# Kernel optimization log

Hardware: AMD Instinct MI355X
Metric: run time of the kernel (lower is better)

Reference implementation:

```python
import jax, jax.numpy as jnp
import numpy as np

B, N, F = 512, 64, 64
ROBOT_DIM, HUMAN_DIM, HID = 9, 5, 128
K = 3  # Chebyshev order


def setup_inputs() -> dict:
    key = jax.random.key(0)
    ks = jax.random.split(key, 16)
    # complete directed graph without self loops, shared across the batch
    src, dst = np.nonzero(~np.eye(N, dtype=bool))
    edge_index = jnp.asarray(np.stack([src, dst]), dtype=jnp.int32)  # [2, E]
    s = 0.05
    return {
        "robot_x": jax.random.normal(ks[0], (B, 1, ROBOT_DIM), jnp.float32),
        "human_x": jax.random.normal(ks[1], (B, N - 1, HUMAN_DIM), jnp.float32),
        "edge_index": edge_index,
        "wr1_w": jax.random.normal(ks[2], (ROBOT_DIM, HID), jnp.float32) * s,
        "wr1_b": jax.random.normal(ks[3], (HID,), jnp.float32) * s,
        "wr2_w": jax.random.normal(ks[4], (HID, F), jnp.float32) * s,
        "wr2_b": jax.random.normal(ks[5], (F,), jnp.float32) * s,
        "wh1_w": jax.random.normal(ks[6], (HUMAN_DIM, HID), jnp.float32) * s,
        "wh1_b": jax.random.normal(ks[7], (HID,), jnp.float32) * s,
        "wh2_w": jax.random.normal(ks[8], (HID, F), jnp.float32) * s,
        "wh2_b": jax.random.normal(ks[9], (F,), jnp.float32) * s,
        "cheb_w": jax.random.normal(ks[10], (K, F, F), jnp.float32) * s,
        "cheb_b": jax.random.normal(ks[11], (F,), jnp.float32) * s,
    }


def reference(robot_x, human_x, edge_index, wr1_w, wr1_b, wr2_w, wr2_b,
              wh1_w, wh1_b, wh2_w, wh2_b, cheb_w, cheb_b):
    # MLP embeddings with last_relu=True
    r = jax.nn.relu(robot_x @ wr1_w + wr1_b)
    r = jax.nn.relu(r @ wr2_w + wr2_b)            # [B, 1, F]
    h = jax.nn.relu(human_x @ wh1_w + wh1_b)
    h = jax.nn.relu(h @ wh2_w + wh2_b)            # [B, N-1, F]
    X = jnp.concatenate([r, h], axis=1)           # [B, N, F]

    src, dst = edge_index[0], edge_index[1]
    n = X.shape[1]
    # PyG ChebConv sym-normalized scaled Laplacian with lambda_max=2:
    # L_hat = -D^{-1/2} A D^{-1/2}  (edge weights all ones, no self loops)
    deg = jax.ops.segment_sum(jnp.ones(src.shape[0], X.dtype), src, num_segments=n)
    dinv = jnp.where(deg > 0, deg ** -0.5, 0.0)
    w = -(dinv[src] * dinv[dst])                  # [E]

    def prop(x):  # x: [B, N, F] -> L_hat @ x per batch via gather/scatter
        msg = x[:, src, :] * w[None, :, None]     # [B, E, F]
        return jnp.zeros_like(x).at[:, dst, :].add(msg)

    Tx0 = X
    Tx1 = prop(X)
    Tx2 = 2.0 * prop(Tx1) - Tx0
    Tx = jnp.stack([Tx0, Tx1, Tx2], axis=0)       # [K, B, N, F]
    out = jnp.einsum("kbnf,kfo->bno", Tx, cheb_w) + cheb_b
    return out[:, 0, :]                           # robot node output [B, F]
```

## Files before the change

kernel.cpp:

```cpp
#include <hip/hip_runtime.h>


#define BDIM 256

typedef __attribute__((ext_vector_type(8))) short bf16x8;
typedef __attribute__((ext_vector_type(4))) float f32x4;

static __device__ __forceinline__ unsigned short f2bf(float f) {
    unsigned int u = __float_as_uint(f);
    u += 0x7FFF + ((u >> 16) & 1);
    return (unsigned short)(u >> 16);
}

__global__ __launch_bounds__(256, 2) void dgcrnn_mfma(
    const float* __restrict__ robot_x,
    const float* __restrict__ human_x,
    const float* __restrict__ wr1, const float* __restrict__ wr1_b,
    const float* __restrict__ wr2, const float* __restrict__ wr2_b,
    const float* __restrict__ wh1, const float* __restrict__ wh1_b,
    const float* __restrict__ wh2, const float* __restrict__ wh2_b,
    const float* __restrict__ cw,  const float* __restrict__ cb,
    float* __restrict__ out)
{
    __shared__ float x_lds[324];
    __shared__ float wh1_l[768];
    __shared__ float wh2b_l[64], wr2b_l[64], cb_l[64];
    __shared__ float rrow[128];
    __shared__ __align__(16) unsigned int wh2T[4096];
    __shared__ __align__(16) short fragA[8192];
    __shared__ __align__(16) float rp_lds[1024];
    __shared__ float hpart[256];

    const int t    = threadIdx.x;
    const int b    = blockIdx.x;
    const int l    = t & 63;
    const int w    = t >> 6;
    const int oq   = t & 15;
    const int o0   = oq * 4;
    const int fgrp = t >> 4;

    float4 wr2q[8];
    #pragma unroll
    for (int j = 0; j < 8; ++j)
        wr2q[j] = *(const float4*)&wr2[(fgrp * 8 + j) * 64 + o0];
    float wr1c[9], wr1bb = 0.f;
    if (t < 128) {
        #pragma unroll
        for (int i = 0; i < 9; ++i) wr1c[i] = wr1[i * 128 + t];
        wr1bb = wr1_b[t];
    }

    for (int i = t; i < 324; i += BDIM)
        x_lds[i] = (i < 9) ? robot_x[b * 9 + i] : human_x[b * 315 + (i - 9)];
    for (int i = t; i < 768; i += BDIM)
        wh1_l[i] = (i < 640) ? wh1[i] : wh1_b[i - 640];
    if (t < 64) { wh2b_l[t] = wh2_b[t]; wr2b_l[t] = wr2_b[t]; cb_l[t] = cb[t]; }
    #pragma unroll
    for (int kk = 0; kk < 4; ++kk) {
        int kp = fgrp * 4 + kk;
        float4 e = *(const float4*)&wh2[(2 * kp) * 64 + o0];
        float4 d = *(const float4*)&wh2[(2 * kp + 1) * 64 + o0];
        #pragma unroll
        for (int c = 0; c < 4; ++c) {
            int o = o0 + c;
            unsigned int wv = (unsigned int)f2bf((&e.x)[c])
                            | ((unsigned int)f2bf((&d.x)[c]) << 16);
            wh2T[o * 64 + (kp ^ ((o & 15) << 2))] = wv;
        }
    }
    __syncthreads();

    {
        const int k0 = ((t >> 6) & 3) * 32 + ((t >> 4) & 3) * 8;
        float wv[5][8], bias8[8];
        #pragma unroll
        for (int j = 0; j < 8; ++j) bias8[j] = wh1_l[640 + k0 + j];
        #pragma unroll
        for (int i = 0; i < 5; ++i)
            #pragma unroll
            for (int j = 0; j < 8; ++j) wv[i][j] = wh1_l[i * 128 + k0 + j];
        #pragma unroll
        for (int s = 0; s < 4; ++s) {
            int slot = s * 256 + t;
            int row  = (s << 4) | (t & 15);
            bf16x8 v;
            #pragma unroll
            for (int j = 0; j < 8; ++j) v[j] = 0;
            if (row != 63) {
                float a8[8];
                #pragma unroll
                for (int j = 0; j < 8; ++j) a8[j] = bias8[j];
                #pragma unroll
                for (int i = 0; i < 5; ++i) {
                    float xv = x_lds[9 + row * 5 + i];
                    #pragma unroll
                    for (int j = 0; j < 8; ++j) a8[j] = fmaf(xv, wv[i][j], a8[j]);
                }
                #pragma unroll
                for (int j = 0; j < 8; ++j) v[j] = (short)f2bf(fmaxf(a8[j], 0.f));
            }
            *reinterpret_cast<bf16x8*>(&fragA[slot * 8]) = v;
        }
    }
    if (t < 128) {
        float a = wr1bb;
        #pragma unroll
        for (int i = 0; i < 9; ++i) a = fmaf(x_lds[i], wr1c[i], a);
        rrow[t] = fmaxf(a, 0.f);
    }
    __syncthreads();

    {
        const int c = l & 15, g = l >> 4, mt = w;
        bf16x8 af[4];
        #pragma unroll
        for (int kt = 0; kt < 4; ++kt)
            af[kt] = *reinterpret_cast<const bf16x8*>(&fragA[((mt * 4 + kt) * 64 + l) * 8]);
        #pragma unroll
        for (int nt = 0; nt < 4; ++nt) {
            const int o = nt * 16 + c;
            f32x4 acc = {0.f, 0.f, 0.f, 0.f};
            #pragma unroll
            for (int kt = 0; kt < 4; ++kt) {
                int kw0 = kt * 16 + g * 4;
                bf16x8 bfv = *reinterpret_cast<const bf16x8*>(
                    &wh2T[o * 64 + (kw0 ^ (c << 2))]);
                acc = __builtin_amdgcn_mfma_f32_16x16x32_bf16(af[kt], bfv, acc, 0, 0, 0);
            }
            float bias = wh2b_l[o];
            float s4 = 0.f;
            #pragma unroll
            for (int reg = 0; reg < 4; ++reg) {
                int node = mt * 16 + g * 4 + reg;
                float hv = fmaxf(acc[reg] + bias, 0.f);
                s4 += (node == 63) ? 0.f : hv;
            }
            s4 += __shfl_xor(s4, 16, 64);
            s4 += __shfl_xor(s4, 32, 64);
            if (g == 0) hpart[mt * 64 + o] = s4;
        }
    }

    {
        float4 rp = {0.f, 0.f, 0.f, 0.f};
        #pragma unroll
        for (int j = 0; j < 8; ++j) {
            float hv = rrow[fgrp * 8 + j];
            rp.x = fmaf(hv, wr2q[j].x, rp.x);
            rp.y = fmaf(hv, wr2q[j].y, rp.y);
            rp.z = fmaf(hv, wr2q[j].z, rp.z);
            rp.w = fmaf(hv, wr2q[j].w, rp.w);
        }
        *(float4*)&rp_lds[fgrp * 64 + o0] = rp;
    }

    float4 cwq[4][3];
    #pragma unroll
    for (int ff = 0; ff < 4; ++ff)
        #pragma unroll
        for (int k = 0; k < 3; ++k)
            cwq[ff][k] = *(const float4*)&cw[k * 4096 + (fgrp * 4 + ff) * 64 + o0];
    __syncthreads();

    {
        const float c1 = 1.0f / 63.0f;
        const float c2 = 2.0f / 3969.0f - 1.0f;
        const float c3 = 124.0f / 3969.0f;
        float4 a4 = {0.f, 0.f, 0.f, 0.f};
        #pragma unroll
        for (int ff = 0; ff < 4; ++ff) {
            int f = fgrp * 4 + ff;
            float rsum = wr2b_l[f];
            #pragma unroll
            for (int kg = 0; kg < 16; ++kg) rsum += rp_lds[kg * 64 + f];
            float rv = fmaxf(rsum, 0.f);
            float sv = rv + hpart[f] + hpart[64 + f] + hpart[128 + f] + hpart[192 + f];
            #pragma unroll
            for (int c = 0; c < 4; ++c) {
                float w0  = (&cwq[ff][0].x)[c];
                float w1  = (&cwq[ff][1].x)[c];
                float w2v = (&cwq[ff][2].x)[c];
                (&a4.x)[c] += rv * (w0 + c1 * w1 + c2 * w2v)
                            + sv * (c3 * w2v - c1 * w1);
            }
        }
        float* out_part = reinterpret_cast<float*>(fragA);
        *(float4*)&out_part[fgrp * 64 + o0] = a4;
    }
    __syncthreads();

    if (t < 64) {
        const float* out_part = reinterpret_cast<const float*>(fragA);
        float a = cb_l[t];
        #pragma unroll
        for (int kg = 0; kg < 16; ++kg) a += out_part[kg * 64 + t];
        out[b * 64 + t] = a;
    }
}

extern "C" void kernel_launch(void* const* d_in, const int* in_sizes, int n_in,
                              void* d_out, int out_size, void* d_ws, size_t ws_size,
                              hipStream_t stream) {
    const float* robot_x = (const float*)d_in[0];
    const float* human_x = (const float*)d_in[1];
    const float* wr1   = (const float*)d_in[3];
    const float* wr1_b = (const float*)d_in[4];
    const float* wr2   = (const float*)d_in[5];
    const float* wr2_b = (const float*)d_in[6];
    const float* wh1   = (const float*)d_in[7];
    const float* wh1_b = (const float*)d_in[8];
    const float* wh2   = (const float*)d_in[9];
    const float* wh2_b = (const float*)d_in[10];
    const float* cw    = (const float*)d_in[11];
    const float* cb    = (const float*)d_in[12];
    float* out = (float*)d_out;

    dgcrnn_mfma<<<512, BDIM, 0, stream>>>(robot_x, human_x,
                                          wr1, wr1_b, wr2, wr2_b,
                                          wh1, wh1_b, wh2, wh2_b,
                                          cw, cb, out);
}
```

Measured before the change: 11.97 us.

## Load wh1 into registers, use packed bf16 convert, shuffle-reduce partial sums

```diff
diff --git a/kernel.cpp b/kernel.cpp
--- a/kernel.cpp
+++ b/kernel.cpp
@@ -5,11 +5,12 @@
 
 typedef __attribute__((ext_vector_type(8))) short bf16x8;
 typedef __attribute__((ext_vector_type(4))) float f32x4;
-
-static __device__ __forceinline__ unsigned short f2bf(float f) {
-    unsigned int u = __float_as_uint(f);
-    u += 0x7FFF + ((u >> 16) & 1);
-    return (unsigned short)(u >> 16);
+typedef __attribute__((ext_vector_type(4))) unsigned int u32x4;
+
+static __device__ __forceinline__ unsigned int cvt_pk_bf16(float lo, float hi) {
+    unsigned int r;
+    asm("v_cvt_pk_bf16_f32 %0, %1, %2" : "=v"(r) : "v"(lo), "v"(hi));
+    return r;
 }
 
 __global__ __launch_bounds__(256, 2) void dgcrnn_mfma(
@@ -23,26 +24,35 @@
     float* __restrict__ out)
 {
     __shared__ float x_lds[324];
-    __shared__ float wh1_l[768];
     __shared__ float wh2b_l[64], wr2b_l[64], cb_l[64];
     __shared__ float rrow[128];
     __shared__ __align__(16) unsigned int wh2T[4096];
     __shared__ __align__(16) short fragA[8192];
-    __shared__ __align__(16) float rp_lds[1024];
+    __shared__ __align__(16) float rp_red[256];
     __shared__ float hpart[256];
 
     const int t    = threadIdx.x;
     const int b    = blockIdx.x;
     const int l    = t & 63;
     const int w    = t >> 6;
-    const int oq   = t & 15;
-    const int o0   = oq * 4;
+    const int o0   = (t & 15) * 4;
     const int fgrp = t >> 4;
 
-    float4 wr2q[8];
+    f32x4 wr2q[8];
     #pragma unroll
     for (int j = 0; j < 8; ++j)
-        wr2q[j] = *(const float4*)&wr2[(fgrp * 8 + j) * 64 + o0];
+        wr2q[j] = *(const f32x4*)&wr2[(fgrp * 8 + j) * 64 + o0];
+
+    const int k0 = ((t >> 6) & 3) * 32 + ((t >> 4) & 3) * 8;
+    f32x4 wv4[10], bias4[2];
+    #pragma unroll
+    for (int i = 0; i < 5; ++i) {
+        wv4[2 * i]     = *(const f32x4*)&wh1[i * 128 + k0];
+        wv4[2 * i + 1] = *(const f32x4*)&wh1[i * 128 + k0 + 4];
+    }
+    bias4[0] = *(const f32x4*)&wh1_b[k0];
+    bias4[1] = *(const f32x4*)&wh1_b[k0 + 4];
+
     float wr1c[9], wr1bb = 0.f;
     if (t < 128) {
         #pragma unroll
@@ -52,55 +62,47 @@
 
     for (int i = t; i < 324; i += BDIM)
         x_lds[i] = (i < 9) ? robot_x[b * 9 + i] : human_x[b * 315 + (i - 9)];
-    for (int i = t; i < 768; i += BDIM)
-        wh1_l[i] = (i < 640) ? wh1[i] : wh1_b[i - 640];
     if (t < 64) { wh2b_l[t] = wh2_b[t]; wr2b_l[t] = wr2_b[t]; cb_l[t] = cb[t]; }
-    #pragma unroll
-    for (int kk = 0; kk < 4; ++kk) {
-        int kp = fgrp * 4 + kk;
-        float4 e = *(const float4*)&wh2[(2 * kp) * 64 + o0];
-        float4 d = *(const float4*)&wh2[(2 * kp + 1) * 64 + o0];
+    {
+        f32x4 e[4], d[4];
+        #pragma unroll
+        for (int kk = 0; kk < 4; ++kk) {
+            int kp = fgrp * 4 + kk;
+            e[kk] = *(const f32x4*)&wh2[(2 * kp) * 64 + o0];
+            d[kk] = *(const f32x4*)&wh2[(2 * kp + 1) * 64 + o0];
+        }
         #pragma unroll
         for (int c = 0; c < 4; ++c) {
             int o = o0 + c;
-            unsigned int wv = (unsigned int)f2bf((&e.x)[c])
-                            | ((unsigned int)f2bf((&d.x)[c]) << 16);
-            wh2T[o * 64 + (kp ^ ((o & 15) << 2))] = wv;
-        }
-    }
-    __syncthreads();
-
-    {
-        const int k0 = ((t >> 6) & 3) * 32 + ((t >> 4) & 3) * 8;
-        float wv[5][8], bias8[8];
-        #pragma unroll
-        for (int j = 0; j < 8; ++j) bias8[j] = wh1_l[640 + k0 + j];
-        #pragma unroll
-        for (int i = 0; i < 5; ++i)
-            #pragma unroll
-            for (int j = 0; j < 8; ++j) wv[i][j] = wh1_l[i * 128 + k0 + j];
-        #pragma unroll
-        for (int s = 0; s < 4; ++s) {
-            int slot = s * 256 + t;
-            int row  = (s << 4) | (t & 15);
-            bf16x8 v;
-            #pragma unroll
-            for (int j = 0; j < 8; ++j) v[j] = 0;
-            if (row != 63) {
-                float a8[8];
+            u32x4 vv;
+            #pragma unroll
+            for (int kk = 0; kk < 4; ++kk) vv[kk] = cvt_pk_bf16(e[kk][c], d[kk][c]);
+            *(u32x4*)&wh2T[o * 64 + ((fgrp * 4) ^ ((o & 15) << 2))] = vv;
+        }
+    }
+    __syncthreads();
+
+    #pragma unroll
+    for (int s = 0; s < 4; ++s) {
+        int slot = s * 256 + t;
+        int row  = (s << 4) | (t & 15);
+        u32x4 vv = {0u, 0u, 0u, 0u};
+        if (row != 63) {
+            float a8[8];
+            #pragma unroll
+            for (int j = 0; j < 8; ++j) a8[j] = bias4[j >> 2][j & 3];
+            #pragma unroll
+            for (int i = 0; i < 5; ++i) {
+                float xv = x_lds[9 + row * 5 + i];
                 #pragma unroll
-                for (int j = 0; j < 8; ++j) a8[j] = bias8[j];
-                #pragma unroll
-                for (int i = 0; i < 5; ++i) {
-                    float xv = x_lds[9 + row * 5 + i];
-                    #pragma unroll
-                    for (int j = 0; j < 8; ++j) a8[j] = fmaf(xv, wv[i][j], a8[j]);
-                }
-                #pragma unroll
-                for (int j = 0; j < 8; ++j) v[j] = (short)f2bf(fmaxf(a8[j], 0.f));
-            }
-            *reinterpret_cast<bf16x8*>(&fragA[slot * 8]) = v;
-        }
+                for (int j = 0; j < 8; ++j)
+                    a8[j] = fmaf(xv, wv4[2 * i + (j >> 2)][j & 3], a8[j]);
+            }
+            #pragma unroll
+            for (int jw = 0; jw < 4; ++jw)
+                vv[jw] = cvt_pk_bf16(fmaxf(a8[2 * jw], 0.f), fmaxf(a8[2 * jw + 1], 0.f));
+        }
+        *(u32x4*)&fragA[slot * 8] = vv;
     }
     if (t < 128) {
         float a = wr1bb;
@@ -141,60 +143,68 @@
         }
     }
 
-    {
-        float4 rp = {0.f, 0.f, 0.f, 0.f};
+    f32x4 cwq[4][3];
+    #pragma unroll
+    for (int ff = 0; ff < 4; ++ff)
+        #pragma unroll
+        for (int k = 0; k < 3; ++k)
+            cwq[ff][k] = *(const f32x4*)&cw[k * 4096 + (fgrp * 4 + ff) * 64 + o0];
+
+    {
+        f32x4 rp = {0.f, 0.f, 0.f, 0.f};
         #pragma unroll
         for (int j = 0; j < 8; ++j) {
             float hv = rrow[fgrp * 8 + j];
-            rp.x = fmaf(hv, wr2q[j].x, rp.x);
-            rp.y = fmaf(hv, wr2q[j].y, rp.y);
-            rp.z = fmaf(hv, wr2q[j].z, rp.z);
-            rp.w = fmaf(hv, wr2q[j].w, rp.w);
-        }
-        *(float4*)&rp_lds[fgrp * 64 + o0] = rp;
-    }
-
-    float4 cwq[4][3];
-    #pragma unroll
-    for (int ff = 0; ff < 4; ++ff)
-        #pragma unroll
-        for (int k = 0; k < 3; ++k)
-            cwq[ff][k] = *(const float4*)&cw[k * 4096 + (fgrp * 4 + ff) * 64 + o0];
+            #pragma unroll
+            for (int c = 0; c < 4; ++c) rp[c] = fmaf(hv, wr2q[j][c], rp[c]);
+        }
+        #pragma unroll
+        for (int c = 0; c < 4; ++c) {
+            float v = rp[c];
+            v += __shfl_xor(v, 16, 64);
+            v += __shfl_xor(v, 32, 64);
+            rp[c] = v;
+        }
+        if (l < 16) *(f32x4*)&rp_red[w * 64 + o0] = rp;
+    }
     __syncthreads();
 
     {
         const float c1 = 1.0f / 63.0f;
         const float c2 = 2.0f / 3969.0f - 1.0f;
         const float c3 = 124.0f / 3969.0f;
-        float4 a4 = {0.f, 0.f, 0.f, 0.f};
+        f32x4 a4 = {0.f, 0.f, 0.f, 0.f};
         #pragma unroll
         for (int ff = 0; ff < 4; ++ff) {
             int f = fgrp * 4 + ff;
-            float rsum = wr2b_l[f];
-            #pragma unroll
-            for (int kg = 0; kg < 16; ++kg) rsum += rp_lds[kg * 64 + f];
+            float rsum = wr2b_l[f] + rp_red[f] + rp_red[64 + f]
+                       + rp_red[128 + f] + rp_red[192 + f];
             float rv = fmaxf(rsum, 0.f);
             float sv = rv + hpart[f] + hpart[64 + f] + hpart[128 + f] + hpart[192 + f];
             #pragma unroll
             for (int c = 0; c < 4; ++c) {
-                float w0  = (&cwq[ff][0].x)[c];
-                float w1  = (&cwq[ff][1].x)[c];
-                float w2v = (&cwq[ff][2].x)[c];
-                (&a4.x)[c] += rv * (w0 + c1 * w1 + c2 * w2v)
-                            + sv * (c3 * w2v - c1 * w1);
-            }
+                float w0  = cwq[ff][0][c];
+                float w1  = cwq[ff][1][c];
+                float w2v = cwq[ff][2][c];
+                a4[c] += rv * (w0 + c1 * w1 + c2 * w2v) + sv * (c3 * w2v - c1 * w1);
+            }
+        }
+        #pragma unroll
+        for (int c = 0; c < 4; ++c) {
+            float v = a4[c];
+            v += __shfl_xor(v, 16, 64);
+            v += __shfl_xor(v, 32, 64);
+            a4[c] = v;
         }
         float* out_part = reinterpret_cast<float*>(fragA);
-        *(float4*)&out_part[fgrp * 64 + o0] = a4;
+        if (l < 16) *(f32x4*)&out_part[w * 64 + o0] = a4;
     }
     __syncthreads();
 
     if (t < 64) {
         const float* out_part = reinterpret_cast<const float*>(fragA);
-        float a = cb_l[t];
-        #pragma unroll
-        for (int kg = 0; kg < 16; ++kg) a += out_part[kg * 64 + t];
-        out[b * 64 + t] = a;
+        out[b * 64 + t] = cb_l[t] + out_part[t] + out_part[64 + t]
+                        + out_part[128 + t] + out_part[192 + t];
     }
 }
 
```

New measurement: 11.44 us. 4.4% less time.
